# Kernel tuning notes

Measured on AMD Instinct MI355X. Metric: run time of the kernel, lower is better.

## Reference

```python
import jax, jax.numpy as jnp
import numpy as np

B, N, F_IN, F_OUT = 1024, 16, 1024, 4096  # n_nodes=16 and n_heads=1 are structurally fixed by the module


def setup_inputs() -> dict:
    key = jax.random.key(0)
    ks = jax.random.split(key, 7)
    s1 = 1.0 / np.sqrt(F_IN)
    s2 = 1.0 / np.sqrt(F_IN * 16)
    return {
        "x": jax.random.normal(ks[0], (B, N, F_IN), jnp.float32),
        "matrix": jax.random.uniform(ks[1], (B, N, N), jnp.float32),
        "W1": jax.random.uniform(ks[2], (F_IN, F_IN), jnp.float32, -s1, s1),
        "b1": jax.random.uniform(ks[3], (F_IN,), jnp.float32, -s1, s1),
        "W_mlp": jax.random.uniform(ks[4], (F_OUT, F_IN * 16), jnp.float32, -s2, s2),
        "b_mlp": jax.random.uniform(ks[5], (F_OUT,), jnp.float32, -s2, s2),
        "a_param": jnp.float32(5.0),
    }


def _l2norm(v):
    # matches F.normalize(p=2, dim=-1, eps=1e-12)
    n = jnp.maximum(jnp.linalg.norm(v, axis=-1, keepdims=True), 1e-12)
    return v / n


def _forward(x, matrix, W1, b1, W_mlp, b_mlp, a_param):
    Bc, n, f = x.shape  # n_heads = 1, n_hidden = f
    wg = x @ W1.T + b1                                    # [B,n,f]
    gs = _l2norm(x)                                       # g_reshaped (H=1)
    gt = _l2norm(wg)                                      # g_transposed
    e = jnp.einsum('bik,bjk->bij', gs, gt)[..., None]     # [B,n,n,1] cosine scores
    eye = jnp.eye(n, dtype=x.dtype)[None, :, :, None]
    e = e * (1.0 + eye * a_param)                         # boost diagonal
    a_scores = e                                          # pre-softmax scores (used below)
    esm = jax.nn.softmax(e, axis=1)                       # softmax over dim=1
    m = matrix[..., None]                                 # [B,n,n,1]
    # MPUGAT message passing
    from_i = jnp.einsum('bitp,btkp->bikp', esm, m)        # [B,n,n,1]
    diag = jnp.einsum('bkkp->bkp', m)                     # diagonal of matrix
    from_j = esm * diag[:, None, :, :]                    # '...jkp,...kkp->...jkp'
    e2 = jnp.einsum('bikp,bjkp->bijp', from_i, from_j)    # [B,n,n,1]
    e2 = 0.5 * (e2 + jnp.transpose(e2, (0, 2, 1, 3)))
    # attention readout with PRE-softmax scores a_scores
    g = x.reshape(Bc, n, 1, f)                            # [B,n,H=1,f]
    attn = jnp.tanh(jnp.einsum('bjhf,bjih->bihf', g, a_scores))  # [B,n,1,f]
    out = attn.reshape(Bc, -1) @ W_mlp.T + b_mlp          # [B,F_OUT]
    out = jnp.broadcast_to(out[:, None, :], (Bc, 16, out.shape[-1]))  # repeat(1,16,1)
    return out, e2, m


def reference(x, matrix, W1, b1, W_mlp, b_mlp, a_param):
    return _forward(x, matrix, W1, b1, W_mlp, b_mlp, a_param)
```

## Files before the change

### kernel.cpp

```cpp
#include <hip/hip_runtime.h>
#include <math.h>

typedef short short8 __attribute__((ext_vector_type(8)));
typedef float f32x4 __attribute__((ext_vector_type(4)));
typedef unsigned short us4 __attribute__((ext_vector_type(4)));
typedef unsigned int u32x4 __attribute__((ext_vector_type(4)));
typedef unsigned short u16;
typedef unsigned int u32;

#define GAS __attribute__((address_space(1)))
#define LAS __attribute__((address_space(3)))

static __device__ __forceinline__ u16 f2bf(float f) {
    union { float f; u32 u; } v; v.f = f;
    u32 r = v.u + 0x7FFFu + ((v.u >> 16) & 1u);
    return (u16)(r >> 16);
}

static __device__ __forceinline__ u32 pk2(float a, float b) {
    return (u32)f2bf(a) | ((u32)f2bf(b) << 16);
}

static __device__ __forceinline__ u32 cvtpk(float lo, float hi) {
    u32 r;
    asm("v_cvt_pk_bf16_f32 %0, %1, %2" : "=v"(r) : "v"(lo), "v"(hi));
    return r;
}

static __device__ __forceinline__ float bf2f(u16 h) {
    union { u32 u; float f; } v; v.u = ((u32)h) << 16;
    return v.f;
}

static __device__ __forceinline__ float ftanh(float v) {
    float t = __expf(-2.0f * fabsf(v));
    float r = (1.0f - t) / (1.0f + t);
    return copysignf(r, v);
}

static __device__ __forceinline__ void gll16(const void* g, void* l) {
    __builtin_amdgcn_global_load_lds((const GAS void*)g, (LAS void*)l, 16, 0, 0);
}

__global__ __launch_bounds__(256) void k_cvt_x(const float* __restrict__ x,
                                               u16* __restrict__ xb,
                                               float* __restrict__ xinv,
                                               const float* __restrict__ W1,
                                               u16* __restrict__ w1b) {
    const int bid = blockIdx.x, t = threadIdx.x;
    if (bid >= 16384) {
        const size_t i = (size_t)(bid - 16384) * 256 + t;
        const f32x4 v = *(const f32x4*)(W1 + 4 * i);
        u32* dst = (u32*)(w1b + 4 * i);
        dst[0] = pk2(v.x, v.y); dst[1] = pk2(v.z, v.w);
        return;
    }
    const int row = bid;
    const f32x4 v = *(const f32x4*)(x + (size_t)row * 1024 + 4 * t);
    u32* dst = (u32*)(xb + (size_t)row * 1024 + 4 * t);
    dst[0] = pk2(v.x, v.y); dst[1] = pk2(v.z, v.w);
    float s = v.x * v.x + v.y * v.y + v.z * v.z + v.w * v.w;
#pragma unroll
    for (int off = 1; off < 64; off <<= 1) s += __shfl_xor(s, off, 64);
    __shared__ float red[4];
    if ((t & 63) == 0) red[t >> 6] = s;
    __syncthreads();
    if (t == 0)
        xinv[row] = 1.0f / fmaxf(sqrtf(red[0] + red[1] + red[2] + red[3]), 1e-12f);
}

#define MFMA16(a, b, c) __builtin_amdgcn_mfma_f32_16x16x32_bf16(a, b, c, 0, 0, 0)
#define SBAR() __builtin_amdgcn_s_barrier()
#define SCHED0() __builtin_amdgcn_sched_barrier(0)
#define VMW6 asm volatile("s_waitcnt vmcnt(6)" ::: "memory")
#define VMW4 asm volatile("s_waitcnt vmcnt(4)" ::: "memory")
#define VMW2 asm volatile("s_waitcnt vmcnt(2)" ::: "memory")
#define VMW0 asm volatile("s_waitcnt vmcnt(0)" ::: "memory")
#define VMW8L asm volatile("s_waitcnt vmcnt(8) lgkmcnt(0)" ::: "memory")
#define VMW0L asm volatile("s_waitcnt vmcnt(0) lgkmcnt(0)" ::: "memory")
#define LGKML asm volatile("s_waitcnt lgkmcnt(0)" ::: "memory")
#define VMNOP do {} while (0)

#define DO_T1(I0, I1, I2, I3, W0, W1M, W2, W3)                                \
  do {                                                                        \
    short8 Af[4][2], Bf0[2][2], Bf1[2][2];                                    \
    _Pragma("unroll") for (int m = 0; m < 4; ++m) {                           \
      Af[m][0] = *(const short8*)(la + rpA[m] + sw0);                         \
      Af[m][1] = *(const short8*)(la + rpA[m] + sw1);                         \
    }                                                                         \
    _Pragma("unroll") for (int n = 0; n < 2; ++n) {                           \
      Bf0[n][0] = *(const short8*)(lb + rpB[n] + sw0);                        \
      Bf0[n][1] = *(const short8*)(lb + rpB[n] + sw1);                        \
    }                                                                         \
    if (I0) { gll16(AG + (saO00 + knxa), danext + ldst);                      \
              gll16(AG + (saO01 + knxa), danext + 4096 + ldst); }             \
    SBAR(); SCHED0();                                                         \
    __builtin_amdgcn_s_setprio(1);                                            \
    _Pragma("unroll") for (int k = 0; k < 2; ++k)                             \
      _Pragma("unroll") for (int m = 0; m < 4; ++m)                           \
        _Pragma("unroll") for (int n = 0; n < 2; ++n)                         \
          acc[m][n] = MFMA16(Af[m][k], Bf0[n][k], acc[m][n]);                 \
    __builtin_amdgcn_s_setprio(0); SCHED0(); W0; SBAR();                      \
    _Pragma("unroll") for (int n = 0; n < 2; ++n) {                           \
      Bf1[n][0] = *(const short8*)(lb + rpB[n + 2] + sw0);                    \
      Bf1[n][1] = *(const short8*)(lb + rpB[n + 2] + sw1);                    \
    }                                                                         \
    if (I1) { gll16(BG + (sbO10 + knxa), dbnext + 8192 + ldst);               \
              gll16(BG + (sbO11 + knxa), dbnext + 8192 + 4096 + ldst); }      \
    SBAR(); SCHED0();                                                         \
    __builtin_amdgcn_s_setprio(1);                                            \
    _Pragma("unroll") for (int k = 0; k < 2; ++k)                             \
      _Pragma("unroll") for (int m = 0; m < 4; ++m)                           \
        _Pragma("unroll") for (int n = 0; n < 2; ++n)                         \
          acc[m][n + 2] = MFMA16(Af[m][k], Bf1[n][k], acc[m][n + 2]);         \
    __builtin_amdgcn_s_setprio(0); SCHED0(); W1M; SBAR();                     \
    _Pragma("unroll") for (int m = 0; m < 4; ++m) {                           \
      Af[m][0] = *(const short8*)(la + rpA[m + 4] + sw0);                     \
      Af[m][1] = *(const short8*)(la + rpA[m + 4] + sw1);                     \
    }                                                                         \
    if (I2) { gll16(AG + (saO10 + knxa), danext + 8192 + ldst);               \
              gll16(AG + (saO11 + knxa), danext + 8192 + 4096 + ldst); }      \
    SBAR(); SCHED0();                                                         \
    __builtin_amdgcn_s_setprio(1);                                            \
    _Pragma("unroll") for (int k = 0; k < 2; ++k)                             \
      _Pragma("unroll") for (int m = 0; m < 4; ++m)                           \
        _Pragma("unroll") for (int n = 0; n < 2; ++n)                         \
          acc[m + 4][n] = MFMA16(Af[m][k], Bf0[n][k], acc[m + 4][n]);         \
    __builtin_amdgcn_s_setprio(0); SCHED0(); W2; SBAR();                      \
    if (I3) { gll16(BG + (sbO00 + knxb), lbw + ldst);                         \
              gll16(BG + (sbO01 + knxb), lbw + 4096 + ldst); }                \
    SBAR(); SCHED0();                                                         \
    __builtin_amdgcn_s_setprio(1);                                            \
    _Pragma("unroll") for (int k = 0; k < 2; ++k)                             \
      _Pragma("unroll") for (int m = 0; m < 4; ++m)                           \
        _Pragma("unroll") for (int n = 0; n < 2; ++n)                         \
          acc[m + 4][n + 2] = MFMA16(Af[m][k], Bf1[n][k], acc[m + 4][n + 2]); \
    __builtin_amdgcn_s_setprio(0); SCHED0(); W3; SBAR();                      \
  } while (0)

#define GEMM1_PROLOGUE()                                                      \
  do {                                                                        \
    gll16(AG + saO00, &LsA[0][0] + ldst);                                     \
    gll16(AG + saO01, &LsA[0][0] + 4096 + ldst);                              \
    gll16(BG + sbO00, &LsB[0][0] + ldst);                                     \
    gll16(BG + sbO01, &LsB[0][0] + 4096 + ldst);                              \
    gll16(BG + sbO10, &LsB[0][0] + 8192 + ldst);                              \
    gll16(BG + sbO11, &LsB[0][0] + 8192 + 4096 + ldst);                       \
    gll16(AG + saO10, &LsA[0][0] + 8192 + ldst);                              \
    gll16(AG + saO11, &LsA[0][0] + 8192 + 4096 + ldst);                       \
    gll16(BG + sbO00 + 64, &LsB[1][0] + ldst);                                \
    gll16(BG + sbO01 + 64, &LsB[1][0] + 4096 + ldst);                         \
    VMW6; SBAR();                                                             \
  } while (0)

#define GT3(ISSA, ISSC, ISSB, KNXA, KNXB, WEND)                               \
  do {                                                                        \
    short8 Af[4][2], Bf0[2][2], Bf1[2][2];                                    \
    if (ISSA) {                                                               \
      gll16(AG + (saO00 + (KNXA)), danext + ldst);                            \
      gll16(AG + (saO01 + (KNXA)), danext + 4096 + ldst);                     \
      gll16(AG + (saO10 + (KNXA)), danext + 8192 + ldst);                     \
      gll16(AG + (saO11 + (KNXA)), danext + 8192 + 4096 + ldst);              \
    }                                                                         \
    _Pragma("unroll") for (int m = 0; m < 4; ++m) {                           \
      Af[m][0] = *(const short8*)(la + rpA[m] + sw0);                         \
      Af[m][1] = *(const short8*)(la + rpA[m] + sw1);                         \
    }                                                                         \
    _Pragma("unroll") for (int n = 0; n < 2; ++n) {                           \
      Bf0[n][0] = *(const short8*)(lb + rpB[n] + sw0);                        \
      Bf0[n][1] = *(const short8*)(lb + rpB[n] + sw1);                        \
      Bf1[n][0] = *(const short8*)(lb + rpB[n + 2] + sw0);                    \
      Bf1[n][1] = *(const short8*)(lb + rpB[n + 2] + sw1);                    \
    }                                                                         \
    __builtin_amdgcn_s_setprio(1);                                            \
    _Pragma("unroll") for (int k = 0; k < 2; ++k)                             \
      _Pragma("unroll") for (int m = 0; m < 4; ++m)                           \
        _Pragma("unroll") for (int n = 0; n < 2; ++n)                         \
          acc[m][n] = MFMA16(Af[m][k], Bf0[n][k], acc[m][n]);                 \
    _Pragma("unroll") for (int k = 0; k < 2; ++k)                             \
      _Pragma("unroll") for (int m = 0; m < 4; ++m)                           \
        _Pragma("unroll") for (int n = 0; n < 2; ++n)                         \
          acc[m][n + 2] = MFMA16(Af[m][k], Bf1[n][k], acc[m][n + 2]);         \
    __builtin_amdgcn_s_setprio(0);                                            \
    _Pragma("unroll") for (int m = 0; m < 4; ++m) {                           \
      Af[m][0] = *(const short8*)(la + rpA[m + 4] + sw0);                     \
      Af[m][1] = *(const short8*)(la + rpA[m + 4] + sw1);                     \
    }                                                                         \
    __builtin_amdgcn_s_setprio(1);                                            \
    _Pragma("unroll") for (int k = 0; k < 2; ++k)                             \
      _Pragma("unroll") for (int m = 0; m < 4; ++m)                           \
        _Pragma("unroll") for (int n = 0; n < 2; ++n)                         \
          acc[m + 4][n] = MFMA16(Af[m][k], Bf0[n][k], acc[m + 4][n]);         \
    __builtin_amdgcn_s_setprio(0);                                            \
    if (ISSC) {                                                               \
      _Pragma("unroll") for (int c = 0; c < 2; ++c) {                         \
        u32x4 wv;                                                             \
        wv.x = cvtpk(bn[2 * c].x, bn[2 * c].y);                               \
        wv.y = cvtpk(bn[2 * c].z, bn[2 * c].w);                               \
        wv.z = cvtpk(bn[2 * c + 1].x, bn[2 * c + 1].y);                       \
        wv.w = cvtpk(bn[2 * c + 1].z, bn[2 * c + 1].w);                       \
        *(u32x4*)(dbnext + c * 4096 + (tid << 3)) = wv;                       \
        if (ISSB) {                                                           \
          bn[2 * c]     = *(const f32x4*)(BGf + bro[c] + (KNXB) + swsrc);     \
          bn[2 * c + 1] = *(const f32x4*)(BGf + bro[c] + (KNXB) + swsrc + 4); \
        }                                                                     \
      }                                                                       \
    }                                                                         \
    __builtin_amdgcn_s_setprio(1);                                            \
    _Pragma("unroll") for (int k = 0; k < 2; ++k)                             \
      _Pragma("unroll") for (int m = 0; m < 4; ++m)                           \
        _Pragma("unroll") for (int n = 0; n < 2; ++n)                         \
          acc[m + 4][n + 2] = MFMA16(Af[m][k], Bf1[n][k], acc[m + 4][n + 2]); \
    __builtin_amdgcn_s_setprio(0);                                            \
    if (ISSC) {                                                               \
      _Pragma("unroll") for (int c = 2; c < 4; ++c) {                         \
        u32x4 wv;                                                             \
        wv.x = cvtpk(bn[2 * c].x, bn[2 * c].y);                               \
        wv.y = cvtpk(bn[2 * c].z, bn[2 * c].w);                               \
        wv.z = cvtpk(bn[2 * c + 1].x, bn[2 * c + 1].y);                       \
        wv.w = cvtpk(bn[2 * c + 1].z, bn[2 * c + 1].w);                       \
        *(u32x4*)(dbnext + c * 4096 + (tid << 3)) = wv;                       \
        if (ISSB) {                                                           \
          bn[2 * c]     = *(const f32x4*)(BGf + bro[c] + (KNXB) + swsrc);     \
          bn[2 * c + 1] = *(const f32x4*)(BGf + bro[c] + (KNXB) + swsrc + 4); \
        }                                                                     \
      }                                                                       \
    }                                                                         \
    SCHED0(); WEND; SBAR();                                                   \
  } while (0)

__global__ __launch_bounds__(512, 2) void k_gemm1_8ph(const u16* __restrict__ AG,
                                                      const u16* __restrict__ BG,
                                                      const float* __restrict__ bias,
                                                      u16* __restrict__ C,
                                                      float* __restrict__ wgn2) {
    __shared__ __align__(16) u16 LsA[2][16384];
    __shared__ __align__(16) u16 LsB[2][16384];
    const int K = 1024, NT = 16;
    const int lin = blockIdx.x;
    const int w = (lin & 7) * 32 + (lin >> 3);
    const int n0 = (w & 3) * 256;
    const int m0 = (w >> 2) * 256;

    const int tid = threadIdx.x, wave = tid >> 6, lane = tid & 63;
    const int lr = lane & 15, kq = lane >> 4;
    const int wr = wave >> 2, wc = wave & 3;

    const int trow = tid >> 3;
    const u32 swsrc = (u32)(((tid & 7) ^ (trow & 7)) * 8);
    const u32 saO00 = (u32)(m0 + 0 + trow) * (u32)K + swsrc;
    const u32 saO01 = (u32)(m0 + 128 + trow) * (u32)K + swsrc;
    const u32 saO10 = (u32)(m0 + 64 + trow) * (u32)K + swsrc;
    const u32 saO11 = (u32)(m0 + 192 + trow) * (u32)K + swsrc;
    const int q0 = trow, q1 = 64 + trow;
    const u32 sbO00 = (u32)(n0 + (q0 >> 5) * 64 + (q0 & 31)) * (u32)K + swsrc;
    const u32 sbO01 = (u32)(n0 + (q1 >> 5) * 64 + (q1 & 31)) * (u32)K + swsrc;
    const u32 sbO10 = (u32)(n0 + (q0 >> 5) * 64 + 32 + (q0 & 31)) * (u32)K + swsrc;
    const u32 sbO11 = (u32)(n0 + (q1 >> 5) * 64 + 32 + (q1 & 31)) * (u32)K + swsrc;
    const u32 ldst = (u32)wave * 512;

    int rpA[8], rpB[4];
#pragma unroll
    for (int mf = 0; mf < 8; ++mf)
        rpA[mf] = ((mf >> 2) * 128 + wr * 64 + (mf & 3) * 16 + lr) << 6;
#pragma unroll
    for (int nf = 0; nf < 4; ++nf)
        rpB[nf] = ((nf >> 1) * 128 + wc * 32 + (nf & 1) * 16 + lr) << 6;
    const int sw0 = ((0 + kq) ^ (lr & 7)) * 8;
    const int sw1 = ((4 + kq) ^ (lr & 7)) * 8;

    f32x4 acc[8][4] = {};

    GEMM1_PROLOGUE();

    int cur = 0;
    for (int T = 0; T < NT - 2; ++T) {
        const u16* la = &LsA[cur][0];
        const u16* lb = &LsB[cur][0];
        u16* danext = &LsA[cur ^ 1][0];
        u16* dbnext = &LsB[cur ^ 1][0];
        u16* lbw = &LsB[cur][0];
        const u32 knxa = (u32)(T + 1) * 64;
        const u32 knxb = (u32)(T + 2) * 64;
        DO_T1(1, 1, 1, 1, VMW6, VMW6, VMW6, VMW6);
        cur ^= 1;
    }
    {
        const u16* la = &LsA[cur][0];
        const u16* lb = &LsB[cur][0];
        u16* danext = &LsA[cur ^ 1][0];
        u16* dbnext = &LsB[cur ^ 1][0];
        u16* lbw = &LsB[cur][0];
        const u32 knxa = (u32)(NT - 1) * 64, knxb = 0;
        (void)knxb;
        DO_T1(1, 1, 1, 0, VMW6, VMW6, VMW6, VMW4);
        cur ^= 1;
    }
    {
        const u16* la = &LsA[cur][0];
        const u16* lb = &LsB[cur][0];
        u16* danext = &LsA[cur ^ 1][0];
        u16* dbnext = &LsB[cur ^ 1][0];
        u16* lbw = &LsB[cur][0];
        const u32 knxa = 0, knxb = 0;
        (void)danext; (void)dbnext; (void)lbw; (void)knxa; (void)knxb;
        DO_T1(0, 0, 0, 0, VMW2, VMW0, VMNOP, VMNOP);
    }

    const int col0 = n0 + wc * 64;
    const int row0 = m0 + wr * 128;
    float bcol[4];
#pragma unroll
    for (int nf = 0; nf < 4; ++nf) bcol[nf] = bias[col0 + nf * 16 + lr];
#pragma unroll
    for (int mf = 0; mf < 8; ++mf) {
#pragma unroll
        for (int r = 0; r < 4; ++r) {
            const int row = row0 + mf * 16 + kq * 4 + r;
            float nrm = 0.f;
#pragma unroll
            for (int nf = 0; nf < 4; ++nf) {
                float v = acc[mf][nf][r] + bcol[nf];
                C[(size_t)row * 1024 + col0 + nf * 16 + lr] = f2bf(v);
                nrm += v * v;
            }
#pragma unroll
            for (int off = 1; off < 16; off <<= 1) nrm += __shfl_xor(nrm, off, 64);
            if (lr == 0) atomicAdd(&wgn2[row], nrm);
        }
    }
}

__global__ __launch_bounds__(512, 2) void k_gemm2_8ph(const u16* __restrict__ AG,
                                                      const float* __restrict__ BGf,
                                                      u16* __restrict__ part) {
    __shared__ __align__(16) u16 LsA[2][16384];
    __shared__ __align__(16) u16 LsB[2][16384];
    const int K = 16384, NT = 64;
    const int lin = blockIdx.x;
    const int w = (lin & 7) * 32 + (lin >> 3);
    const int m0 = (w & 3) * 256;
    const int z = (w >> 2) & 3;
    const int n0 = (w >> 4) * 256;
    const int kbeg = z * 4096;

    const int tid = threadIdx.x, wave = tid >> 6, lane = tid & 63;
    const int lr = lane & 15, kq = lane >> 4;
    const int wr = wave >> 2, wc = wave & 3;

    const int trow = tid >> 3;
    const u32 swsrc = (u32)(((tid & 7) ^ (trow & 7)) * 8);
    const u32 saO00 = (u32)(m0 + 0 + trow) * (u32)K + (u32)kbeg + swsrc;
    const u32 saO01 = (u32)(m0 + 128 + trow) * (u32)K + (u32)kbeg + swsrc;
    const u32 saO10 = (u32)(m0 + 64 + trow) * (u32)K + (u32)kbeg + swsrc;
    const u32 saO11 = (u32)(m0 + 192 + trow) * (u32)K + (u32)kbeg + swsrc;
    const int q0 = trow, q1 = 64 + trow;
    u32 bro[4];
    bro[0] = (u32)(n0 + (q0 >> 5) * 64 + (q0 & 31)) * 16384u + (u32)kbeg;
    bro[1] = (u32)(n0 + (q1 >> 5) * 64 + (q1 & 31)) * 16384u + (u32)kbeg;
    bro[2] = bro[0] + 32u * 16384u;
    bro[3] = bro[1] + 32u * 16384u;
    const u32 ldst = (u32)wave * 512;

    int rpA[8], rpB[4];
#pragma unroll
    for (int mf = 0; mf < 8; ++mf)
        rpA[mf] = ((mf >> 2) * 128 + wr * 64 + (mf & 3) * 16 + lr) << 6;
#pragma unroll
    for (int nf = 0; nf < 4; ++nf)
        rpB[nf] = ((nf >> 1) * 128 + wc * 32 + (nf & 1) * 16 + lr) << 6;
    const int sw0 = ((0 + kq) ^ (lr & 7)) * 8;
    const int sw1 = ((4 + kq) ^ (lr & 7)) * 8;

    f32x4 acc[8][4] = {};
    f32x4 bn[8];

    {
        gll16(AG + saO00, &LsA[0][0] + ldst);
        gll16(AG + saO01, &LsA[0][0] + 4096 + ldst);
        gll16(AG + saO10, &LsA[0][0] + 8192 + ldst);
        gll16(AG + saO11, &LsA[0][0] + 8192 + 4096 + ldst);
#pragma unroll
        for (int c = 0; c < 4; ++c) {
            bn[2 * c]     = *(const f32x4*)(BGf + bro[c] + swsrc);
            bn[2 * c + 1] = *(const f32x4*)(BGf + bro[c] + swsrc + 4);
        }
#pragma unroll
        for (int c = 0; c < 4; ++c) {
            u32x4 wv;
            wv.x = cvtpk(bn[2 * c].x, bn[2 * c].y);
            wv.y = cvtpk(bn[2 * c].z, bn[2 * c].w);
            wv.z = cvtpk(bn[2 * c + 1].x, bn[2 * c + 1].y);
            wv.w = cvtpk(bn[2 * c + 1].z, bn[2 * c + 1].w);
            *(u32x4*)(&LsB[0][0] + c * 4096 + (tid << 3)) = wv;
        }
        asm volatile("s_waitcnt vmcnt(0) lgkmcnt(0)" ::: "memory");
#pragma unroll
        for (int c = 0; c < 4; ++c) {
            bn[2 * c]     = *(const f32x4*)(BGf + bro[c] + 64 + swsrc);
            bn[2 * c + 1] = *(const f32x4*)(BGf + bro[c] + 64 + swsrc + 4);
        }
        SBAR();
    }

    int cur = 0;
    for (int T = 0; T < NT - 2; ++T) {
        const u16* la = &LsA[cur][0];
        const u16* lb = &LsB[cur][0];
        u16* danext = &LsA[cur ^ 1][0];
        u16* dbnext = &LsB[cur ^ 1][0];
        const u32 knxa = (u32)(T + 1) * 64;
        const u32 knxb = (u32)(T + 2) * 64;
        GT3(1, 1, 1, knxa, knxb, VMW8L);
        cur ^= 1;
    }
    {
        const u16* la = &LsA[cur][0];
        const u16* lb = &LsB[cur][0];
        u16* danext = &LsA[cur ^ 1][0];
        u16* dbnext = &LsB[cur ^ 1][0];
        const u32 knxa = 63u * 64, knxb = 0;
        (void)knxb;
        GT3(1, 1, 0, knxa, 0u, VMW0L);
        cur ^= 1;
    }
    {
        const u16* la = &LsA[cur][0];
        const u16* lb = &LsB[cur][0];
        u16* danext = &LsA[cur ^ 1][0];
        u16* dbnext = &LsB[cur ^ 1][0];
        (void)danext; (void)dbnext;
        GT3(0, 0, 0, 0u, 0u, VMNOP);
    }

    u16* po = part + (size_t)z * 4194304ull;
    const int col0 = n0 + wc * 64;
    const int row0 = m0 + wr * 128;
#pragma unroll
    for (int mf = 0; mf < 8; ++mf)
#pragma unroll
        for (int r = 0; r < 4; ++r) {
            const int row = row0 + mf * 16 + kq * 4 + r;
#pragma unroll
            for (int nf = 0; nf < 4; ++nf)
                po[(size_t)row * 4096 + col0 + nf * 16 + lr] = f2bf(acc[mf][nf][r]);
        }
}

__global__ __launch_bounds__(256) void k_batch_attn(const u16* xb,
                                                    const u16* __restrict__ wgb,
                                                    const float* __restrict__ xinv,
                                                    const float* __restrict__ wgn2,
                                                    const float* __restrict__ matrix,
                                                    const float* __restrict__ a_param,
                                                    float* __restrict__ e2_out,
                                                    float* __restrict__ m_out,
                                                    u16* attn_bf) {
    const int b = blockIdx.x, tid = threadIdx.x;
    const int wave = tid >> 6, lane = tid & 63;
    const int j = lane & 15, ig = (lane >> 4) * 4;

    __shared__ float qred[4][64][4];
    __shared__ float esm_l[16 * 17];
    __shared__ float fi_l[16 * 17];
    __shared__ float e2_l[16 * 17];
    __shared__ float m_l[256];
    __shared__ float as_l[256];
    __shared__ u16 xsh[16][256];

    {
        const size_t roff = (size_t)(b * 16 + j) * 1024 + (lane >> 4) * 8 + wave * 256;
        f32x4 acc0 = {}, acc1 = {};
#pragma unroll
        for (int kt = 0; kt < 256; kt += 64) {
            short8 xa0 = *(const short8*)(xb + roff + kt);
            short8 wa0 = *(const short8*)(wgb + roff + kt);
            short8 xa1 = *(const short8*)(xb + roff + kt + 32);
            short8 wa1 = *(const short8*)(wgb + roff + kt + 32);
            acc0 = __builtin_amdgcn_mfma_f32_16x16x32_bf16(xa0, wa0, acc0, 0, 0, 0);
            acc1 = __builtin_amdgcn_mfma_f32_16x16x32_bf16(xa1, wa1, acc1, 0, 0, 0);
        }
#pragma unroll
        for (int r = 0; r < 4; ++r) qred[wave][lane][r] = acc0[r] + acc1[r];
    }
    __syncthreads();

    if (tid < 64) {
        const int l = tid;
        const float inw = 1.0f / fmaxf(sqrtf(wgn2[b * 16 + j]), 1e-12f);
        const float boost = 1.0f + a_param[0];
        float e[4];
#pragma unroll
        for (int r = 0; r < 4; ++r) {
            const int i = ig + r;
            float v = (qred[0][l][r] + qred[1][l][r] + qred[2][l][r] + qred[3][l][r]) *
                      xinv[b * 16 + i] * inw;
            if (i == j) v *= boost;
            e[r] = v;
            as_l[i * 16 + j] = v;
        }
        float mx = fmaxf(fmaxf(e[0], e[1]), fmaxf(e[2], e[3]));
        mx = fmaxf(mx, __shfl_xor(mx, 16, 64));
        mx = fmaxf(mx, __shfl_xor(mx, 32, 64));
        float p[4], s = 0.f;
#pragma unroll
        for (int r = 0; r < 4; ++r) { p[r] = __expf(e[r] - mx); s += p[r]; }
        s += __shfl_xor(s, 16, 64);
        s += __shfl_xor(s, 32, 64);
        const float invs = 1.0f / s;
#pragma unroll
        for (int r = 0; r < 4; ++r) esm_l[(ig + r) * 17 + j] = p[r] * invs;
        const f32x4 mv = *(const f32x4*)(matrix + (size_t)b * 256 + 4 * l);
        *(f32x4*)(m_l + 4 * l) = mv;
        *(f32x4*)(m_out + (size_t)b * 256 + 4 * l) = mv;
    }
    __syncthreads();
    if (tid < 64) {
        float fi[4] = {0, 0, 0, 0};
#pragma unroll
        for (int t = 0; t < 16; ++t) {
            const float mk = m_l[t * 16 + j];
#pragma unroll
            for (int r = 0; r < 4; ++r) fi[r] += esm_l[(ig + r) * 17 + t] * mk;
        }
#pragma unroll
        for (int r = 0; r < 4; ++r) fi_l[(ig + r) * 17 + j] = fi[r];
    }
    __syncthreads();
    if (tid < 64) {
        float e2v[4] = {0, 0, 0, 0};
#pragma unroll
        for (int kk = 0; kk < 16; ++kk) {
            const float wgt = esm_l[j * 17 + kk] * m_l[kk * 16 + kk];
#pragma unroll
            for (int r = 0; r < 4; ++r) e2v[r] += fi_l[(ig + r) * 17 + kk] * wgt;
        }
#pragma unroll
        for (int r = 0; r < 4; ++r) e2_l[(ig + r) * 17 + j] = e2v[r];
    }
    __syncthreads();
    if (tid < 64) {
#pragma unroll
        for (int r = 0; r < 4; ++r) {
            const int i = ig + r;
            e2_out[(size_t)b * 256 + i * 16 + j] =
                0.5f * (e2_l[i * 17 + j] + e2_l[j * 17 + i]);
        }
    }

    const int srow = tid >> 4;
    const int scol = (tid & 15) * 16;
    for (int ch = 0; ch < 4; ++ch) {
        __syncthreads();
        const u16* src = xb + ((size_t)b * 16 + srow) * 1024 + ch * 256 + scol;
        *(short8*)&xsh[srow][scol] = *(const short8*)src;
        *(short8*)&xsh[srow][scol + 8] = *(const short8*)(src + 8);
        __syncthreads();
        float accv[16] = {};
#pragma unroll
        for (int jj = 0; jj < 16; ++jj) {
            const float xv = bf2f(xsh[jj][tid]);
#pragma unroll
            for (int i = 0; i < 16; ++i) accv[i] = fmaf(as_l[jj * 16 + i], xv, accv[i]);
        }
#pragma unroll
        for (int i = 0; i < 16; ++i)
            attn_bf[((size_t)b * 16 + i) * 1024 + ch * 256 + tid] = f2bf(ftanh(accv[i]));
    }
}

__global__ __launch_bounds__(256) void k_bcast(const u16* __restrict__ p,
                                               const float* __restrict__ bias,
                                               float* __restrict__ out) {
    const size_t i = (size_t)blockIdx.x * 256 + threadIdx.x;
    const int o4 = (int)(i & 1023);
    const int b = (int)(i >> 14);
    const size_t src = (size_t)b * 4096 + (size_t)o4 * 4;
    f32x4 r = *(const f32x4*)(bias + (size_t)o4 * 4);
#pragma unroll
    for (int z = 0; z < 4; ++z) {
        us4 v = *(const us4*)(p + (size_t)z * 4194304ull + src);
        r.x += bf2f(v.x); r.y += bf2f(v.y); r.z += bf2f(v.z); r.w += bf2f(v.w);
    }
    *(f32x4*)(out + i * 4) = r;
}

extern "C" void kernel_launch(void* const* d_in, const int* in_sizes, int n_in,
                              void* d_out, int out_size, void* d_ws, size_t ws_size,
                              hipStream_t stream) {
    const float* x      = (const float*)d_in[0];
    const float* matrix = (const float*)d_in[1];
    const float* W1     = (const float*)d_in[2];
    const float* b1     = (const float*)d_in[3];
    const float* W_mlp  = (const float*)d_in[4];
    const float* b_mlp  = (const float*)d_in[5];
    const float* a_par  = (const float*)d_in[6];
    float* out = (float*)d_out;

    char* ws = (char*)d_ws;
    size_t off = 0;
    auto alloc = [&](size_t bytes) {
        char* p = ws + off;
        off += (bytes + 255) & ~(size_t)255;
        return p;
    };
    u16*   x_bf  = (u16*)alloc(16384ull * 1024 * 2);
    u16*   wg_bf = (u16*)alloc(16384ull * 1024 * 2);
    u16*   w1_bf = (u16*)alloc(1024ull * 1024 * 2);
    float* xinv  = (float*)alloc(16384ull * 4);
    float* wgn2  = (float*)alloc(16384ull * 4);
    u16*   attn_bf = x_bf;
    u16*   part    = wg_bf;
    float* e2_out = out + 67108864ull;
    float* m_out  = out + 67371008ull;

    hipMemsetAsync(wgn2, 0, 16384 * 4, stream);
    k_cvt_x<<<17408, 256, 0, stream>>>(x, x_bf, xinv, W1, w1_bf);
    k_gemm1_8ph<<<256, 512, 0, stream>>>(x_bf, w1_bf, b1, wg_bf, wgn2);
    k_batch_attn<<<1024, 256, 0, stream>>>(x_bf, wg_bf, xinv, wgn2, matrix, a_par,
                                           e2_out, m_out, attn_bf);
    k_gemm2_8ph<<<256, 512, 0, stream>>>(attn_bf, W_mlp, part);
    k_bcast<<<65536, 256, 0, stream>>>(part, b_mlp, out);
}
```

Measured before the change: 318.4 us.

## Simplify GEMM1 main loop to single-barrier double-buffered tile pipeline

Replaces the four-phase interleaved GEMM1 loop, which had barriers between each MFMA quarter and split global-to-LDS loads, with a simpler scheme. Each tile now issues all eight next-tile loads up front, runs all 32 MFMAs, then waits for all loads and hits one barrier. This removes many barriers and waitcnt points per tile. In exchange it loses the finer-grained overlap and the two-ahead B prefetch of the old schedule, so memory latency may be exposed at the per-tile vmcnt(0) wait.

```diff
diff --git a/kernel.cpp b/kernel.cpp
--- a/kernel.cpp
+++ b/kernel.cpp
@@ -72,18 +72,24 @@
 #define MFMA16(a, b, c) __builtin_amdgcn_mfma_f32_16x16x32_bf16(a, b, c, 0, 0, 0)
 #define SBAR() __builtin_amdgcn_s_barrier()
 #define SCHED0() __builtin_amdgcn_sched_barrier(0)
-#define VMW6 asm volatile("s_waitcnt vmcnt(6)" ::: "memory")
-#define VMW4 asm volatile("s_waitcnt vmcnt(4)" ::: "memory")
-#define VMW2 asm volatile("s_waitcnt vmcnt(2)" ::: "memory")
 #define VMW0 asm volatile("s_waitcnt vmcnt(0)" ::: "memory")
 #define VMW8L asm volatile("s_waitcnt vmcnt(8) lgkmcnt(0)" ::: "memory")
 #define VMW0L asm volatile("s_waitcnt vmcnt(0) lgkmcnt(0)" ::: "memory")
-#define LGKML asm volatile("s_waitcnt lgkmcnt(0)" ::: "memory")
 #define VMNOP do {} while (0)
 
-#define DO_T1(I0, I1, I2, I3, W0, W1M, W2, W3)                                \
+#define GT1S(ISS, KNX, WEND)                                                  \
   do {                                                                        \
     short8 Af[4][2], Bf0[2][2], Bf1[2][2];                                    \
+    if (ISS) {                                                                \
+      gll16(AG + (saO00 + (KNX)), danext + ldst);                             \
+      gll16(AG + (saO01 + (KNX)), danext + 4096 + ldst);                      \
+      gll16(AG + (saO10 + (KNX)), danext + 8192 + ldst);                      \
+      gll16(AG + (saO11 + (KNX)), danext + 8192 + 4096 + ldst);               \
+      gll16(BG + (sbO00 + (KNX)), dbnext + ldst);                             \
+      gll16(BG + (sbO01 + (KNX)), dbnext + 4096 + ldst);                      \
+      gll16(BG + (sbO10 + (KNX)), dbnext + 8192 + ldst);                      \
+      gll16(BG + (sbO11 + (KNX)), dbnext + 8192 + 4096 + ldst);               \
+    }                                                                         \
     _Pragma("unroll") for (int m = 0; m < 4; ++m) {                           \
       Af[m][0] = *(const short8*)(la + rpA[m] + sw0);                         \
       Af[m][1] = *(const short8*)(la + rpA[m] + sw1);                         \
@@ -91,66 +97,34 @@
     _Pragma("unroll") for (int n = 0; n < 2; ++n) {                           \
       Bf0[n][0] = *(const short8*)(lb + rpB[n] + sw0);                        \
       Bf0[n][1] = *(const short8*)(lb + rpB[n] + sw1);                        \
-    }                                                                         \
-    if (I0) { gll16(AG + (saO00 + knxa), danext + ldst);                      \
-              gll16(AG + (saO01 + knxa), danext + 4096 + ldst); }             \
-    SBAR(); SCHED0();                                                         \
-    __builtin_amdgcn_s_setprio(1);                                            \
-    _Pragma("unroll") for (int k = 0; k < 2; ++k)                             \
-      _Pragma("unroll") for (int m = 0; m < 4; ++m)                           \
-        _Pragma("unroll") for (int n = 0; n < 2; ++n)                         \
-          acc[m][n] = MFMA16(Af[m][k], Bf0[n][k], acc[m][n]);                 \
-    __builtin_amdgcn_s_setprio(0); SCHED0(); W0; SBAR();                      \
-    _Pragma("unroll") for (int n = 0; n < 2; ++n) {                           \
       Bf1[n][0] = *(const short8*)(lb + rpB[n + 2] + sw0);                    \
       Bf1[n][1] = *(const short8*)(lb + rpB[n + 2] + sw1);                    \
     }                                                                         \
-    if (I1) { gll16(BG + (sbO10 + knxa), dbnext + 8192 + ldst);               \
-              gll16(BG + (sbO11 + knxa), dbnext + 8192 + 4096 + ldst); }      \
-    SBAR(); SCHED0();                                                         \
     __builtin_amdgcn_s_setprio(1);                                            \
     _Pragma("unroll") for (int k = 0; k < 2; ++k)                             \
       _Pragma("unroll") for (int m = 0; m < 4; ++m)                           \
         _Pragma("unroll") for (int n = 0; n < 2; ++n)                         \
+          acc[m][n] = MFMA16(Af[m][k], Bf0[n][k], acc[m][n]);                 \
+    _Pragma("unroll") for (int k = 0; k < 2; ++k)                             \
+      _Pragma("unroll") for (int m = 0; m < 4; ++m)                           \
+        _Pragma("unroll") for (int n = 0; n < 2; ++n)                         \
           acc[m][n + 2] = MFMA16(Af[m][k], Bf1[n][k], acc[m][n + 2]);         \
-    __builtin_amdgcn_s_setprio(0); SCHED0(); W1M; SBAR();                     \
+    __builtin_amdgcn_s_setprio(0);                                            \
     _Pragma("unroll") for (int m = 0; m < 4; ++m) {                           \
       Af[m][0] = *(const short8*)(la + rpA[m + 4] + sw0);                     \
       Af[m][1] = *(const short8*)(la + rpA[m + 4] + sw1);                     \
     }                                                                         \
-    if (I2) { gll16(AG + (saO10 + knxa), danext + 8192 + ldst);               \
-              gll16(AG + (saO11 + knxa), danext + 8192 + 4096 + ldst); }      \
-    SBAR(); SCHED0();                                                         \
     __builtin_amdgcn_s_setprio(1);                                            \
     _Pragma("unroll") for (int k = 0; k < 2; ++k)                             \
       _Pragma("unroll") for (int m = 0; m < 4; ++m)                           \
         _Pragma("unroll") for (int n = 0; n < 2; ++n)                         \
           acc[m + 4][n] = MFMA16(Af[m][k], Bf0[n][k], acc[m + 4][n]);         \
-    __builtin_amdgcn_s_setprio(0); SCHED0(); W2; SBAR();                      \
-    if (I3) { gll16(BG + (sbO00 + knxb), lbw + ldst);                         \
-              gll16(BG + (sbO01 + knxb), lbw + 4096 + ldst); }                \
-    SBAR(); SCHED0();                                                         \
-    __builtin_amdgcn_s_setprio(1);                                            \
     _Pragma("unroll") for (int k = 0; k < 2; ++k)                             \
       _Pragma("unroll") for (int m = 0; m < 4; ++m)                           \
         _Pragma("unroll") for (int n = 0; n < 2; ++n)                         \
           acc[m + 4][n + 2] = MFMA16(Af[m][k], Bf1[n][k], acc[m + 4][n + 2]); \
-    __builtin_amdgcn_s_setprio(0); SCHED0(); W3; SBAR();                      \
-  } while (0)
-
-#define GEMM1_PROLOGUE()                                                      \
-  do {                                                                        \
-    gll16(AG + saO00, &LsA[0][0] + ldst);                                     \
-    gll16(AG + saO01, &LsA[0][0] + 4096 + ldst);                              \
-    gll16(BG + sbO00, &LsB[0][0] + ldst);                                     \
-    gll16(BG + sbO01, &LsB[0][0] + 4096 + ldst);                              \
-    gll16(BG + sbO10, &LsB[0][0] + 8192 + ldst);                              \
-    gll16(BG + sbO11, &LsB[0][0] + 8192 + 4096 + ldst);                       \
-    gll16(AG + saO10, &LsA[0][0] + 8192 + ldst);                              \
-    gll16(AG + saO11, &LsA[0][0] + 8192 + 4096 + ldst);                       \
-    gll16(BG + sbO00 + 64, &LsB[1][0] + ldst);                                \
-    gll16(BG + sbO01 + 64, &LsB[1][0] + 4096 + ldst);                         \
-    VMW6; SBAR();                                                             \
+    __builtin_amdgcn_s_setprio(0);                                            \
+    SCHED0(); WEND; SBAR();                                                   \
   } while (0)
 
 #define GT3(ISSA, ISSC, ISSB, KNXA, KNXB, WEND)                               \
@@ -271,18 +245,25 @@
 
     f32x4 acc[8][4] = {};
 
-    GEMM1_PROLOGUE();
+    gll16(AG + saO00, &LsA[0][0] + ldst);
+    gll16(AG + saO01, &LsA[0][0] + 4096 + ldst);
+    gll16(AG + saO10, &LsA[0][0] + 8192 + ldst);
+    gll16(AG + saO11, &LsA[0][0] + 8192 + 4096 + ldst);
+    gll16(BG + sbO00, &LsB[0][0] + ldst);
+    gll16(BG + sbO01, &LsB[0][0] + 4096 + ldst);
+    gll16(BG + sbO10, &LsB[0][0] + 8192 + ldst);
+    gll16(BG + sbO11, &LsB[0][0] + 8192 + 4096 + ldst);
+    VMW0;
+    SBAR();
 
     int cur = 0;
-    for (int T = 0; T < NT - 2; ++T) {
+    for (int T = 0; T < NT - 1; ++T) {
         const u16* la = &LsA[cur][0];
         const u16* lb = &LsB[cur][0];
         u16* danext = &LsA[cur ^ 1][0];
         u16* dbnext = &LsB[cur ^ 1][0];
-        u16* lbw = &LsB[cur][0];
-        const u32 knxa = (u32)(T + 1) * 64;
-        const u32 knxb = (u32)(T + 2) * 64;
-        DO_T1(1, 1, 1, 1, VMW6, VMW6, VMW6, VMW6);
+        const u32 knx = (u32)(T + 1) * 64;
+        GT1S(1, knx, VMW0);
         cur ^= 1;
     }
     {
@@ -290,21 +271,8 @@
         const u16* lb = &LsB[cur][0];
         u16* danext = &LsA[cur ^ 1][0];
         u16* dbnext = &LsB[cur ^ 1][0];
-        u16* lbw = &LsB[cur][0];
-        const u32 knxa = (u32)(NT - 1) * 64, knxb = 0;
-        (void)knxb;
-        DO_T1(1, 1, 1, 0, VMW6, VMW6, VMW6, VMW4);
-        cur ^= 1;
-    }
-    {
-        const u16* la = &LsA[cur][0];
-        const u16* lb = &LsB[cur][0];
-        u16* danext = &LsA[cur ^ 1][0];
-        u16* dbnext = &LsB[cur ^ 1][0];
-        u16* lbw = &LsB[cur][0];
-        const u32 knxa = 0, knxb = 0;
-        (void)danext; (void)dbnext; (void)lbw; (void)knxa; (void)knxb;
-        DO_T1(0, 0, 0, 0, VMW2, VMW0, VMNOP, VMNOP);
+        (void)danext; (void)dbnext;
+        GT1S(0, 0u, VMNOP);
     }
 
     const int col0 = n0 + wc * 64;
@@ -419,9 +387,7 @@
         const u16* lb = &LsB[cur][0];
         u16* danext = &LsA[cur ^ 1][0];
         u16* dbnext = &LsB[cur ^ 1][0];
-        const u32 knxa = 63u * 64, knxb = 0;
-        (void)knxb;
-        GT3(1, 1, 0, knxa, 0u, VMW0L);
+        GT3(1, 1, 0, 63u * 64, 0u, VMW0L);
         cur ^= 1;
     }
     {
```

New measurement: 323.2 us. About the same (+1.5%).
